# Optimization experiments

Measured on AMD Instinct MI355X. Metric: run time of the kernel, lower is better.

The kernel has to match this reference:

```python
import jax, jax.numpy as jnp
import numpy as np

N_DISEASE, N_GENE, E, D = 20000, 100000, 2000000, 128


def setup_inputs() -> dict:
    key = jax.random.key(0)
    ks = jax.random.split(key, 12)
    s = 0.05  # weight scale keeps exp(logstd) well-behaved
    return {
        "x_disease": jax.random.normal(ks[0], (N_DISEASE, D), jnp.float32),
        "x_gene": jax.random.normal(ks[1], (N_GENE, D), jnp.float32),
        "edge_src": jax.random.randint(ks[2], (E,), 0, N_DISEASE, jnp.int32),
        "edge_dst": jax.random.randint(ks[3], (E,), 0, N_GENE, jnp.int32),
        "eps": jax.random.normal(ks[4], (N_GENE, D), jnp.float32),
        # SAGEConv (disease->gene): lin_l (on aggregated neighbors, with bias), lin_r (on dst root, no bias)
        "W_l": jax.random.normal(ks[5], (D, D), jnp.float32) * s,
        "b_l": jnp.zeros((D,), jnp.float32),
        "W_r": jax.random.normal(ks[6], (D, D), jnp.float32) * s,
        # fc_mu_gene / fc_logvar_gene
        "mu_W": jax.random.normal(ks[7], (D, D), jnp.float32) * s,
        "mu_b": jnp.zeros((D,), jnp.float32),
        "lv_W": jax.random.normal(ks[8], (D, D), jnp.float32) * s,
        "lv_b": jnp.zeros((D,), jnp.float32),
    }


def reference(x_disease, x_gene, edge_src, edge_dst, eps,
              W_l, b_l, W_r, mu_W, mu_b, lv_W, lv_b):
    # --- SAGEConv('disease' -> 'gene'), aggr='mean' ---
    msg = x_disease[edge_src]                                   # [E, D] gather
    summed = jax.ops.segment_sum(msg, edge_dst, num_segments=N_GENE)   # [N_gene, D]
    cnt = jax.ops.segment_sum(jnp.ones((msg.shape[0],), msg.dtype), edge_dst,
                              num_segments=N_GENE)
    mean = summed / jnp.maximum(cnt, 1.0)[:, None]
    h_gene = mean @ W_l + b_l + x_gene @ W_r                    # [N_gene, D]
    # (HeteroConv aggr='mean' is identity: only one relation targets 'gene')

    # --- mu / logstd heads + VGAE reparametrize ---
    mu = h_gene @ mu_W + mu_b
    logstd = h_gene @ lv_W + lv_b
    z = mu + eps * jnp.exp(logstd)
    return z
```

## Files before the change

kernel.cpp:

```cpp
#include <hip/hip_runtime.h>
#include <math.h>

#define D 128
#define ST 64
#define GBIN 256
#define CAP 6144
#define BCAP 8192
#define BK2_E 16
#define NBMAX 512

typedef short bf16x8 __attribute__((ext_vector_type(8)));
typedef short bf16x4 __attribute__((ext_vector_type(4)));
typedef float f32x4 __attribute__((ext_vector_type(4)));
typedef float f32x2 __attribute__((ext_vector_type(2)));

#if __has_builtin(__builtin_amdgcn_cvt_pk_f32_fp8) && __has_builtin(__builtin_amdgcn_cvt_pk_fp8_f32)
#define HW_FP8 1
#else
#define HW_FP8 0
#endif

__device__ inline unsigned short f2bf(float f) {
    union { float f; unsigned u; } v; v.f = f;
    unsigned r = v.u + 0x7fff + ((v.u >> 16) & 1);
    return (unsigned short)(r >> 16);
}
__device__ inline float bf2f(unsigned short u) {
    union { unsigned u; float f; } v; v.u = ((unsigned)u) << 16;
    return v.f;
}

__device__ inline unsigned f2fp8(float f) {
    union { float f; unsigned u; } v; v.f = f;
    unsigned s = v.u >> 31;
    unsigned mag = v.u & 0x7fffffffu;
    if (mag > 0x43E00000u) mag = 0x43E00000u;
    unsigned r = mag + 0x7FFFFu + ((mag >> 20) & 1);
    int e = (int)(r >> 23) - 120;
    unsigned out;
    if (e <= 0) {
        float ax;
        { union { unsigned u; float f; } w; w.u = mag; ax = w.f; }
        int m = (int)(ax * 512.0f + 0.5f);
        out = (m > 7) ? 8u : (unsigned)m;
    } else {
        out = ((unsigned)e << 3) | ((r >> 20) & 7);
    }
    return (s << 7) | out;
}
__device__ inline float fp8dec(unsigned b) {
    unsigned s = b >> 7, em = b & 0x7f;
    union { unsigned u; float f; } w;
    w.u = (em << 20) + 0x3C000000u;
    float v = (em >= 8) ? w.f : (float)(int)em * 0.001953125f;
    return s ? -v : v;
}

__device__ inline unsigned pack_fp8x4(float4 a) {
#if HW_FP8
    int r = __builtin_amdgcn_cvt_pk_fp8_f32(a.x, a.y, 0, false);
    r = __builtin_amdgcn_cvt_pk_fp8_f32(a.z, a.w, r, true);
    return (unsigned)r;
#else
    return f2fp8(a.x) | (f2fp8(a.y) << 8) | (f2fp8(a.z) << 16) | (f2fp8(a.w) << 24);
#endif
}
__device__ inline void unpack_fp8x4_add(unsigned w, f32x2* acc01, f32x2* acc23) {
#if HW_FP8
    f32x2 p0 = __builtin_amdgcn_cvt_pk_f32_fp8(w, false);
    f32x2 p1 = __builtin_amdgcn_cvt_pk_f32_fp8(w, true);
    *acc01 += p0;
    *acc23 += p1;
#else
    f32x2 p0 = { fp8dec(w & 0xff), fp8dec((w >> 8) & 0xff) };
    f32x2 p1 = { fp8dec((w >> 16) & 0xff), fp8dec((w >> 24) & 0xff) };
    *acc01 += p0;
    *acc23 += p1;
#endif
}

__global__ void init_bcur_kernel(int* __restrict__ bcur, int nbin)
{
    int b = blockIdx.x * blockDim.x + threadIdx.x;
    if (b < nbin) bcur[b] = b * BCAP;
}

__global__ __launch_bounds__(256) void bucket2_kernel(
    const int* __restrict__ esrc, const int* __restrict__ edst,
    int* __restrict__ bcur, unsigned* __restrict__ pairs2, int E, int nbin)
{
    __shared__ int lcount[NBMAX];
    __shared__ int lbase[NBMAX];
    int t = threadIdx.x;
    const int batch = 256 * BK2_E;
    for (long long base = (long long)blockIdx.x * batch; base < E;
         base += (long long)gridDim.x * batch) {
        for (int b = t; b < nbin; b += 256) lcount[b] = 0;
        __syncthreads();
        int bb[BK2_E], rr[BK2_E];
        unsigned pv[BK2_E];
        #pragma unroll
        for (int j = 0; j < BK2_E; ++j) {
            int e = (int)base + t + j * 256;
            bb[j] = -1;
            if (e < E) {
                int dd = __builtin_nontemporal_load(&edst[e]);
                int ss = __builtin_nontemporal_load(&esrc[e]);
                int bin = dd >> 8;
                bb[j] = bin;
                pv[j] = ((unsigned)(dd & (GBIN - 1)) << 16) | (unsigned)ss;
                rr[j] = atomicAdd(&lcount[bin], 1);
            }
        }
        __syncthreads();
        for (int b = t; b < nbin; b += 256)
            lbase[b] = lcount[b] ? atomicAdd(&bcur[b], lcount[b]) : 0;
        __syncthreads();
        #pragma unroll
        for (int j = 0; j < BK2_E; ++j)
            if (bb[j] >= 0) {
                int pos = lbase[bb[j]] + rr[j];
                if (pos < (bb[j] + 1) * BCAP)
                    pairs2[pos] = pv[j];
            }
        __syncthreads();
    }
}

__global__ __launch_bounds__(256) void fill3b_kernel(
    const unsigned* __restrict__ pairs2, const int* __restrict__ bcur,
    int* __restrict__ offs, int* __restrict__ oend,
    unsigned short* __restrict__ csr, int ngene)
{
    __shared__ int lhist[GBIN];
    __shared__ int lofs[GBIN];
    __shared__ int lcur[GBIN];
    __shared__ unsigned short stage[CAP];
    int b = blockIdx.x;
    int t = threadIdx.x;
    int g0 = b * GBIN;
    int ng = min(GBIN, ngene - g0);
    int sb = b * BCAP;
    int se = min(bcur[b], sb + BCAP);
    int n = se - sb;

    lhist[t] = 0;
    __syncthreads();
    for (int i = sb + t; i < se; i += 256)
        atomicAdd(&lhist[pairs2[i] >> 16], 1);
    __syncthreads();
    int v = lhist[t];
    lofs[t] = v;
    __syncthreads();
    for (int off = 1; off < GBIN; off <<= 1) {
        int add = (t >= off) ? lofs[t - off] : 0;
        __syncthreads();
        lofs[t] += add;
        __syncthreads();
    }
    int myofs = lofs[t] - v;
    lcur[t] = myofs;
    if (t < ng) {
        offs[g0 + t] = sb + myofs;
        oend[g0 + t] = sb + myofs + v;
    }
    __syncthreads();

    if (n <= CAP) {
        for (int i = sb + t; i < se; i += 256) {
            unsigned u = pairs2[i];
            int pos = atomicAdd(&lcur[u >> 16], 1);
            stage[pos] = (unsigned short)(u & 0xffffu);
        }
        __syncthreads();
        for (int i = t; i < n; i += 256)
            csr[sb + i] = stage[i];
    } else {
        for (int i = sb + t; i < se; i += 256) {
            unsigned u = pairs2[i];
            int pos = atomicAdd(&lcur[u >> 16], 1);
            csr[sb + pos] = (unsigned short)(u & 0xffffu);
        }
    }
}

__global__ __launch_bounds__(256) void cvt_kernel(
    const float* __restrict__ xd, unsigned char* __restrict__ xdb8, int nxd,
    const float* __restrict__ w0, const float* __restrict__ w1,
    const float* __restrict__ w2, const float* __restrict__ w3,
    unsigned short* __restrict__ t0, unsigned short* __restrict__ t1,
    unsigned short* __restrict__ t2, unsigned short* __restrict__ t3)
{
    int b = blockIdx.x;
    if (b < nxd) {
        int i = b * 256 + threadIdx.x;
        float4 a = ((const float4*)xd)[i * 2];
        float4 c = ((const float4*)xd)[i * 2 + 1];
        ((uint2*)xdb8)[i] = make_uint2(pack_fp8x4(a), pack_fp8x4(c));
    } else {
        int m = b - nxd;
        const float* src = m == 0 ? w0 : m == 1 ? w1 : m == 2 ? w2 : w3;
        unsigned short* dst = m == 0 ? t0 : m == 1 ? t1 : m == 2 ? t2 : t3;
        for (int idx = threadIdx.x; idx < D * D; idx += 256) {
            int k = idx >> 7, n = idx & 127;
            dst[n * D + k] = f2bf(src[idx]);
        }
    }
}

__global__ __launch_bounds__(256, 6) void gather_kernel(
    const int* __restrict__ offs, const int* __restrict__ oend,
    const unsigned short* __restrict__ csr,
    const unsigned char* __restrict__ xdb8, unsigned short* __restrict__ meanb,
    int ngene)
{
    int tid = threadIdx.x;
    int r = tid >> 4, c = tid & 15;
    int row = blockIdx.x * 16 + r;
    if (row >= ngene) return;
    int beg = offs[row], end = oend[row];
    const uint2* tab = (const uint2*)xdb8;
    f32x2 a0[4] = {{0,0},{0,0},{0,0},{0,0}};
    f32x2 a1[4] = {{0,0},{0,0},{0,0},{0,0}};
    int i = beg;
    for (; i + 2 <= end; i += 2) {
        int s0 = csr[i], s1 = csr[i + 1];
        uint2 v0 = tab[s0 * 16 + c];
        uint2 v1 = tab[s1 * 16 + c];
        unpack_fp8x4_add(v0.x, &a0[0], &a0[1]);
        unpack_fp8x4_add(v0.y, &a0[2], &a0[3]);
        unpack_fp8x4_add(v1.x, &a1[0], &a1[1]);
        unpack_fp8x4_add(v1.y, &a1[2], &a1[3]);
    }
    if (i < end) {
        int s0 = csr[i];
        uint2 v0 = tab[s0 * 16 + c];
        unpack_fp8x4_add(v0.x, &a0[0], &a0[1]);
        unpack_fp8x4_add(v0.y, &a0[2], &a0[3]);
    }
    float inv = 1.0f / fmaxf((float)(end - beg), 1.0f);
    bf16x8 o;
    #pragma unroll
    for (int j = 0; j < 4; ++j) {
        f32x2 s = a0[j] + a1[j];
        o[j * 2]     = (short)f2bf(s[0] * inv);
        o[j * 2 + 1] = (short)f2bf(s[1] * inv);
    }
    ((bf16x8*)meanb)[row * 16 + c] = o;
}

__global__ __launch_bounds__(512, 2) void hz_kernel(
    const unsigned short* __restrict__ meanb, const float* __restrict__ xg,
    const float* __restrict__ eps,
    const unsigned short* __restrict__ WlT, const unsigned short* __restrict__ WrT,
    const unsigned short* __restrict__ muT, const unsigned short* __restrict__ lvT,
    const float* __restrict__ bl, const float* __restrict__ mub,
    const float* __restrict__ lvb, float* __restrict__ z, int ngene, int nst)
{
    __shared__ unsigned short mean_s[ST][132];
    __shared__ unsigned short xg_s[ST][132];
    __shared__ unsigned short h_s[ST][132];

    int tid = threadIdx.x;
    int wave = tid >> 6;
    int lane = tid & 63;
    int lr = lane & 15;
    int lg = lane >> 4;
    int cb = wave * 16;
    int nb = cb + lg * 4;

    int row0 = tid >> 4, c0 = tid & 15;
    int row1 = row0 + 32;

    float4 bl4 = *(const float4*)&bl[nb];
    float4 mb4 = *(const float4*)&mub[nb];
    float4 lb4 = *(const float4*)&lvb[nb];

    bf16x8 pm0, pm1;
    f32x4 px00, px01, px10, px11;

#define LOAD_TILE(stv) do {                                              \
        int rb_ = (stv) * ST;                                            \
        int g0_ = rb_ + row0; if (g0_ >= ngene) g0_ = ngene - 1;         \
        int g1_ = rb_ + row1; if (g1_ >= ngene) g1_ = ngene - 1;         \
        pm0 = *(const bf16x8*)&meanb[(size_t)g0_ * D + c0 * 8];          \
        pm1 = *(const bf16x8*)&meanb[(size_t)g1_ * D + c0 * 8];          \
        const f32x4* xp0_ = (const f32x4*)&xg[(size_t)g0_ * D + c0 * 8]; \
        const f32x4* xp1_ = (const f32x4*)&xg[(size_t)g1_ * D + c0 * 8]; \
        px00 = xp0_[0]; px01 = xp0_[1];                                  \
        px10 = xp1_[0]; px11 = xp1_[1];                                  \
    } while (0)

    if (blockIdx.x < nst) LOAD_TILE(blockIdx.x);

    for (int st = blockIdx.x; st < nst; st += gridDim.x) {
        int rowbase = st * ST;

        f32x4 epr[4];
        #pragma unroll
        for (int rt = 0; rt < 4; ++rt) {
            int orow = rowbase + rt * 16 + lr;
            if (orow >= ngene) orow = ngene - 1;
            epr[rt] = *(const f32x4*)&eps[(size_t)orow * D + nb];
        }

        {
            *(bf16x8*)&mean_s[row0][c0 * 8] = pm0;
            *(bf16x8*)&mean_s[row1][c0 * 8] = pm1;
            bf16x8 v;
            v[0] = (short)f2bf(px00[0]); v[1] = (short)f2bf(px00[1]);
            v[2] = (short)f2bf(px00[2]); v[3] = (short)f2bf(px00[3]);
            v[4] = (short)f2bf(px01[0]); v[5] = (short)f2bf(px01[1]);
            v[6] = (short)f2bf(px01[2]); v[7] = (short)f2bf(px01[3]);
            *(bf16x8*)&xg_s[row0][c0 * 8] = v;
            v[0] = (short)f2bf(px10[0]); v[1] = (short)f2bf(px10[1]);
            v[2] = (short)f2bf(px10[2]); v[3] = (short)f2bf(px10[3]);
            v[4] = (short)f2bf(px11[0]); v[5] = (short)f2bf(px11[1]);
            v[6] = (short)f2bf(px11[2]); v[7] = (short)f2bf(px11[3]);
            *(bf16x8*)&xg_s[row1][c0 * 8] = v;
        }
        __syncthreads();

        int stn = st + gridDim.x;
        if (stn < nst) LOAD_TILE(stn);

        {
            bf16x8 wl[4], wr[4];
            #pragma unroll
            for (int kc = 0; kc < 4; ++kc) {
                int koff = kc * 32 + lg * 8;
                wl[kc] = *(const bf16x8*)&WlT[(cb + lr) * D + koff];
                wr[kc] = *(const bf16x8*)&WrT[(cb + lr) * D + koff];
            }
            #pragma unroll
            for (int rt = 0; rt < 4; ++rt) {
                int r0 = rt * 16 + lr;
                f32x4 accm = {bl4.x, bl4.y, bl4.z, bl4.w};
                f32x4 accx = {0.f, 0.f, 0.f, 0.f};
                #pragma unroll
                for (int kc = 0; kc < 4; ++kc) {
                    int koff = kc * 32 + lg * 8;
                    bf16x8 am = *(const bf16x8*)&mean_s[r0][koff];
                    bf16x8 ax = *(const bf16x8*)&xg_s[r0][koff];
                    accm = __builtin_amdgcn_mfma_f32_16x16x32_bf16(wl[kc], am, accm, 0, 0, 0);
                    accx = __builtin_amdgcn_mfma_f32_16x16x32_bf16(wr[kc], ax, accx, 0, 0, 0);
                }
                bf16x4 hp;
                #pragma unroll
                for (int r = 0; r < 4; ++r) hp[r] = (short)f2bf(accm[r] + accx[r]);
                *(bf16x4*)&h_s[r0][nb] = hp;
            }
        }
        __syncthreads();

        {
            bf16x8 mu[4], lv[4];
            #pragma unroll
            for (int kc = 0; kc < 4; ++kc) {
                int koff = kc * 32 + lg * 8;
                mu[kc] = *(const bf16x8*)&muT[(cb + lr) * D + koff];
                lv[kc] = *(const bf16x8*)&lvT[(cb + lr) * D + koff];
            }
            #pragma unroll
            for (int rt = 0; rt < 4; ++rt) {
                int r0 = rt * 16 + lr;
                f32x4 zm = {mb4.x, mb4.y, mb4.z, mb4.w};
                f32x4 zl = {lb4.x, lb4.y, lb4.z, lb4.w};
                #pragma unroll
                for (int kc = 0; kc < 4; ++kc) {
                    int koff = kc * 32 + lg * 8;
                    bf16x8 ah = *(const bf16x8*)&h_s[r0][koff];
                    zm = __builtin_amdgcn_mfma_f32_16x16x32_bf16(mu[kc], ah, zm, 0, 0, 0);
                    zl = __builtin_amdgcn_mfma_f32_16x16x32_bf16(lv[kc], ah, zl, 0, 0, 0);
                }
                int orow = rowbase + r0;
                if (orow < ngene) {
                    float4 zo;
                    zo.x = zm[0] + epr[rt][0] * __expf(zl[0]);
                    zo.y = zm[1] + epr[rt][1] * __expf(zl[1]);
                    zo.z = zm[2] + epr[rt][2] * __expf(zl[2]);
                    zo.w = zm[3] + epr[rt][3] * __expf(zl[3]);
                    *(float4*)&z[(size_t)orow * D + nb] = zo;
                }
            }
        }
        __syncthreads();
    }
#undef LOAD_TILE
}

extern "C" void kernel_launch(void* const* d_in, const int* in_sizes, int n_in,
                              void* d_out, int out_size, void* d_ws, size_t ws_size,
                              hipStream_t stream)
{
    const float* xd  = (const float*)d_in[0];
    const float* xg  = (const float*)d_in[1];
    const int* esrc  = (const int*)d_in[2];
    const int* edst  = (const int*)d_in[3];
    const float* eps = (const float*)d_in[4];
    const float* Wl  = (const float*)d_in[5];
    const float* bl  = (const float*)d_in[6];
    const float* Wr  = (const float*)d_in[7];
    const float* muW = (const float*)d_in[8];
    const float* mub = (const float*)d_in[9];
    const float* lvW = (const float*)d_in[10];
    const float* lvb = (const float*)d_in[11];

    int E = in_sizes[2];
    int ndis = in_sizes[0] / D;
    int ngene = in_sizes[1] / D;
    int nbin = (ngene + GBIN - 1) / GBIN;

    char* p = (char*)d_ws;
    int* offs = (int*)p;  p += (size_t)ngene * 4;
    int* oend = (int*)p;  p += (size_t)ngene * 4;
    int* bcur = (int*)p;  p += NBMAX * 4;
    p = (char*)(((size_t)p + 255) & ~(size_t)255);
    unsigned char* xdb8 = (unsigned char*)p;  p += (size_t)ndis * D;
    unsigned short* WlT = (unsigned short*)p; p += D * D * 2;
    unsigned short* WrT = (unsigned short*)p; p += D * D * 2;
    unsigned short* muT = (unsigned short*)p; p += D * D * 2;
    unsigned short* lvT = (unsigned short*)p; p += D * D * 2;
    p = (char*)(((size_t)p + 255) & ~(size_t)255);
    unsigned* pairs2 = (unsigned*)p;          p += (size_t)nbin * BCAP * 4;
    unsigned short* csr_src = (unsigned short*)p; p += (size_t)nbin * BCAP * 2;
    p = (char*)(((size_t)p + 255) & ~(size_t)255);
    unsigned short* meanb = (unsigned short*)p;

    init_bcur_kernel<<<(nbin + 255) / 256, 256, 0, stream>>>(bcur, nbin);
    bucket2_kernel<<<512, 256, 0, stream>>>(esrc, edst, bcur, pairs2, E, nbin);
    fill3b_kernel<<<nbin, 256, 0, stream>>>(pairs2, bcur, offs, oend, csr_src, ngene);

    int nxd = ndis * D / 8 / 256;
    cvt_kernel<<<nxd + 4, 256, 0, stream>>>(xd, xdb8, nxd,
                                            Wl, Wr, muW, lvW, WlT, WrT, muT, lvT);

    gather_kernel<<<(ngene + 15) / 16, 256, 0, stream>>>(offs, oend, csr_src,
                                                         xdb8, meanb, ngene);

    int nst = (ngene + ST - 1) / ST;
    hz_kernel<<<512, 512, 0, stream>>>(meanb, xg, eps, WlT, WrT, muT, lvT,
                                       bl, mub, lvb, (float*)d_out, ngene, nst);
}
```

Baseline: 139.8 us.

## Fuse bucketing with conversion, memset bin counters, unroll gather, nontemporal stores

Merges the edge-bucketing kernel and the fp8/bf16 conversion kernel into a single launch with extra blocks. The bin-cursor init kernel becomes a hipMemsetAsync, so cursors now hold relative counts. The gather loop is unrolled to four independent neighbor loads and accumulators for more memory-level parallelism. The final z stores become nontemporal. Together these aim to cut launch overhead and latency stalls, at the cost of more registers in gather and a change in cursor semantics.

```diff
diff --git a/kernel.cpp b/kernel.cpp
--- a/kernel.cpp
+++ b/kernel.cpp
@@ -8,6 +8,7 @@
 #define BCAP 8192
 #define BK2_E 16
 #define NBMAX 512
+#define BK_BLOCKS 512
 
 typedef short bf16x8 __attribute__((ext_vector_type(8)));
 typedef short bf16x4 __attribute__((ext_vector_type(4)));
@@ -79,22 +80,41 @@
 #endif
 }
 
-__global__ void init_bcur_kernel(int* __restrict__ bcur, int nbin)
+__global__ __launch_bounds__(256) void bucket2_cvt_kernel(
+    const int* __restrict__ esrc, const int* __restrict__ edst,
+    int* __restrict__ bcur, unsigned* __restrict__ pairs2, int E, int nbin,
+    const float* __restrict__ xd, unsigned char* __restrict__ xdb8, int nxd,
+    const float* __restrict__ w0, const float* __restrict__ w1,
+    const float* __restrict__ w2, const float* __restrict__ w3,
+    unsigned short* __restrict__ t0, unsigned short* __restrict__ t1,
+    unsigned short* __restrict__ t2, unsigned short* __restrict__ t3)
 {
-    int b = blockIdx.x * blockDim.x + threadIdx.x;
-    if (b < nbin) bcur[b] = b * BCAP;
-}
-
-__global__ __launch_bounds__(256) void bucket2_kernel(
-    const int* __restrict__ esrc, const int* __restrict__ edst,
-    int* __restrict__ bcur, unsigned* __restrict__ pairs2, int E, int nbin)
-{
+    int blk = blockIdx.x;
+    if (blk >= BK_BLOCKS) {
+        int b = blk - BK_BLOCKS;
+        if (b < nxd) {
+            int i = b * 256 + threadIdx.x;
+            float4 a = ((const float4*)xd)[i * 2];
+            float4 c = ((const float4*)xd)[i * 2 + 1];
+            ((uint2*)xdb8)[i] = make_uint2(pack_fp8x4(a), pack_fp8x4(c));
+        } else {
+            int m = b - nxd;
+            const float* src = m == 0 ? w0 : m == 1 ? w1 : m == 2 ? w2 : w3;
+            unsigned short* dst = m == 0 ? t0 : m == 1 ? t1 : m == 2 ? t2 : t3;
+            for (int idx = threadIdx.x; idx < D * D; idx += 256) {
+                int k = idx >> 7, n = idx & 127;
+                dst[n * D + k] = f2bf(src[idx]);
+            }
+        }
+        return;
+    }
+
     __shared__ int lcount[NBMAX];
     __shared__ int lbase[NBMAX];
     int t = threadIdx.x;
     const int batch = 256 * BK2_E;
-    for (long long base = (long long)blockIdx.x * batch; base < E;
-         base += (long long)gridDim.x * batch) {
+    for (long long base = (long long)blk * batch; base < E;
+         base += (long long)BK_BLOCKS * batch) {
         for (int b = t; b < nbin; b += 256) lcount[b] = 0;
         __syncthreads();
         int bb[BK2_E], rr[BK2_E];
@@ -119,9 +139,9 @@
         #pragma unroll
         for (int j = 0; j < BK2_E; ++j)
             if (bb[j] >= 0) {
-                int pos = lbase[bb[j]] + rr[j];
-                if (pos < (bb[j] + 1) * BCAP)
-                    pairs2[pos] = pv[j];
+                int rel = lbase[bb[j]] + rr[j];
+                if (rel < BCAP)
+                    pairs2[(size_t)bb[j] * BCAP + rel] = pv[j];
             }
         __syncthreads();
     }
@@ -140,9 +160,9 @@
     int t = threadIdx.x;
     int g0 = b * GBIN;
     int ng = min(GBIN, ngene - g0);
+    int n = min(bcur[b], BCAP);
     int sb = b * BCAP;
-    int se = min(bcur[b], sb + BCAP);
-    int n = se - sb;
+    int se = sb + n;
 
     lhist[t] = 0;
     __syncthreads();
@@ -180,30 +200,6 @@
             unsigned u = pairs2[i];
             int pos = atomicAdd(&lcur[u >> 16], 1);
             csr[sb + pos] = (unsigned short)(u & 0xffffu);
-        }
-    }
-}
-
-__global__ __launch_bounds__(256) void cvt_kernel(
-    const float* __restrict__ xd, unsigned char* __restrict__ xdb8, int nxd,
-    const float* __restrict__ w0, const float* __restrict__ w1,
-    const float* __restrict__ w2, const float* __restrict__ w3,
-    unsigned short* __restrict__ t0, unsigned short* __restrict__ t1,
-    unsigned short* __restrict__ t2, unsigned short* __restrict__ t3)
-{
-    int b = blockIdx.x;
-    if (b < nxd) {
-        int i = b * 256 + threadIdx.x;
-        float4 a = ((const float4*)xd)[i * 2];
-        float4 c = ((const float4*)xd)[i * 2 + 1];
-        ((uint2*)xdb8)[i] = make_uint2(pack_fp8x4(a), pack_fp8x4(c));
-    } else {
-        int m = b - nxd;
-        const float* src = m == 0 ? w0 : m == 1 ? w1 : m == 2 ? w2 : w3;
-        unsigned short* dst = m == 0 ? t0 : m == 1 ? t1 : m == 2 ? t2 : t3;
-        for (int idx = threadIdx.x; idx < D * D; idx += 256) {
-            int k = idx >> 7, n = idx & 127;
-            dst[n * D + k] = f2bf(src[idx]);
         }
     }
 }
@@ -222,17 +218,25 @@
     const uint2* tab = (const uint2*)xdb8;
     f32x2 a0[4] = {{0,0},{0,0},{0,0},{0,0}};
     f32x2 a1[4] = {{0,0},{0,0},{0,0},{0,0}};
+    f32x2 a2[4] = {{0,0},{0,0},{0,0},{0,0}};
+    f32x2 a3[4] = {{0,0},{0,0},{0,0},{0,0}};
     int i = beg;
-    for (; i + 2 <= end; i += 2) {
-        int s0 = csr[i], s1 = csr[i + 1];
+    for (; i + 4 <= end; i += 4) {
+        int s0 = csr[i], s1 = csr[i + 1], s2 = csr[i + 2], s3 = csr[i + 3];
         uint2 v0 = tab[s0 * 16 + c];
         uint2 v1 = tab[s1 * 16 + c];
+        uint2 v2 = tab[s2 * 16 + c];
+        uint2 v3 = tab[s3 * 16 + c];
         unpack_fp8x4_add(v0.x, &a0[0], &a0[1]);
         unpack_fp8x4_add(v0.y, &a0[2], &a0[3]);
         unpack_fp8x4_add(v1.x, &a1[0], &a1[1]);
         unpack_fp8x4_add(v1.y, &a1[2], &a1[3]);
-    }
-    if (i < end) {
+        unpack_fp8x4_add(v2.x, &a2[0], &a2[1]);
+        unpack_fp8x4_add(v2.y, &a2[2], &a2[3]);
+        unpack_fp8x4_add(v3.x, &a3[0], &a3[1]);
+        unpack_fp8x4_add(v3.y, &a3[2], &a3[3]);
+    }
+    for (; i < end; ++i) {
         int s0 = csr[i];
         uint2 v0 = tab[s0 * 16 + c];
         unpack_fp8x4_add(v0.x, &a0[0], &a0[1]);
@@ -242,7 +246,7 @@
     bf16x8 o;
     #pragma unroll
     for (int j = 0; j < 4; ++j) {
-        f32x2 s = a0[j] + a1[j];
+        f32x2 s = (a0[j] + a1[j]) + (a2[j] + a3[j]);
         o[j * 2]     = (short)f2bf(s[0] * inv);
         o[j * 2 + 1] = (short)f2bf(s[1] * inv);
     }
@@ -375,12 +379,12 @@
                 }
                 int orow = rowbase + r0;
                 if (orow < ngene) {
-                    float4 zo;
-                    zo.x = zm[0] + epr[rt][0] * __expf(zl[0]);
-                    zo.y = zm[1] + epr[rt][1] * __expf(zl[1]);
-                    zo.z = zm[2] + epr[rt][2] * __expf(zl[2]);
-                    zo.w = zm[3] + epr[rt][3] * __expf(zl[3]);
-                    *(float4*)&z[(size_t)orow * D + nb] = zo;
+                    f32x4 zo;
+                    zo[0] = zm[0] + epr[rt][0] * __expf(zl[0]);
+                    zo[1] = zm[1] + epr[rt][1] * __expf(zl[1]);
+                    zo[2] = zm[2] + epr[rt][2] * __expf(zl[2]);
+                    zo[3] = zm[3] + epr[rt][3] * __expf(zl[3]);
+                    __builtin_nontemporal_store(zo, (f32x4*)&z[(size_t)orow * D + nb]);
                 }
             }
         }
@@ -427,13 +431,14 @@
     p = (char*)(((size_t)p + 255) & ~(size_t)255);
     unsigned short* meanb = (unsigned short*)p;
 
-    init_bcur_kernel<<<(nbin + 255) / 256, 256, 0, stream>>>(bcur, nbin);
-    bucket2_kernel<<<512, 256, 0, stream>>>(esrc, edst, bcur, pairs2, E, nbin);
+    hipMemsetAsync(bcur, 0, NBMAX * sizeof(int), stream);
+
+    int nxd = ndis * D / 8 / 256;
+    bucket2_cvt_kernel<<<BK_BLOCKS + nxd + 4, 256, 0, stream>>>(
+        esrc, edst, bcur, pairs2, E, nbin,
+        xd, xdb8, nxd, Wl, Wr, muW, lvW, WlT, WrT, muT, lvT);
+
     fill3b_kernel<<<nbin, 256, 0, stream>>>(pairs2, bcur, offs, oend, csr_src, ngene);
-
-    int nxd = ndis * D / 8 / 256;
-    cvt_kernel<<<nxd + 4, 256, 0, stream>>>(xd, xdb8, nxd,
-                                            Wl, Wr, muW, lvW, WlT, WrT, muT, lvT);
 
     gather_kernel<<<(ngene + 15) / 16, 256, 0, stream>>>(offs, oend, csr_src,
                                                          xdb8, meanb, ngene);
```

Result: faster. 127.2 us (-9.0%).
